# Kernel optimization log

Hardware: AMD Instinct MI355X
Metric: run time of the kernel (lower is better)

## Reference

```python
import jax, jax.numpy as jnp
import numpy as np

N_NODES = 20000
N_EDGES = 160000
D_IN = 512
D_OUT = 64


def _propagate(x, src, dst, num_nodes):
    # SLPropagate with add_self_loops=False, normalize=False:
    # out[dst] += x[src]  (plain sum aggregation over incoming edges)
    return jax.ops.segment_sum(x[src], dst, num_segments=num_nodes)


def setup_inputs() -> dict:
    key = jax.random.key(0)
    k1, k2, k3, k4 = jax.random.split(key, 4)
    x = jax.random.normal(k1, (N_NODES, D_IN), dtype=jnp.float32)
    edge_index = jax.random.randint(k2, (2, N_EDGES), 0, N_NODES, dtype=jnp.int64)
    # torch.nn.Linear default init scale ~ 1/sqrt(fan_in)
    s = 1.0 / np.sqrt(D_IN)
    W1 = jax.random.uniform(k3, (D_IN, D_IN), dtype=jnp.float32, minval=-s, maxval=s)
    W2 = jax.random.uniform(k4, (D_OUT, D_IN), dtype=jnp.float32, minval=-s, maxval=s)
    return {"x": x, "edge_index": edge_index, "W1": W1, "W2": W2}


def reference(x, edge_index, W1, W2):
    num_nodes = x.shape[0]
    src, dst = edge_index[0], edge_index[1]
    h = _propagate(x, src, dst, num_nodes)          # [N, D_IN]
    h = jax.nn.relu(jnp.einsum('nd,ed->ne', h, W1))  # lin1 (no bias) + relu
    h = _propagate(h, src, dst, num_nodes)          # [N, D_IN]
    h = jnp.einsum('nd,od->no', h, W2)              # lin2 (no bias) -> [N, D_OUT]
    return jax.nn.log_softmax(h, axis=1)
```

## Files before the change

kernel.cpp:

```cpp
#include <hip/hip_runtime.h>

#define D 512
#define DOUT 64

typedef __bf16 bf16x8 __attribute__((ext_vector_type(8)));
typedef float floatx4 __attribute__((ext_vector_type(4)));

__device__ __forceinline__ void async_cp16(const void* g, void* lds) {
    __builtin_amdgcn_global_load_lds(
        (__attribute__((address_space(1))) void*)(void*)g,
        (__attribute__((address_space(3))) void*)lds, 16, 0, 0);
}

__global__ __launch_bounds__(256) void prep_kernel(
        int* __restrict__ deg, int nN, int zeroBlocks,
        const float* __restrict__ x, __bf16* __restrict__ xb, int xN8,
        const float* __restrict__ W1, __bf16* __restrict__ w1b, int w1N8,
        const float* __restrict__ W2, __bf16* __restrict__ w2b, int w2N8) {
    int b = blockIdx.x;
    if (b < zeroBlocks) {
        int i4 = b * 1024 + threadIdx.x * 4;
        if (i4 + 3 < nN) *(int4*)(deg + i4) = make_int4(0, 0, 0, 0);
        else {
            if (i4 + 0 < nN) deg[i4 + 0] = 0;
            if (i4 + 1 < nN) deg[i4 + 1] = 0;
            if (i4 + 2 < nN) deg[i4 + 2] = 0;
        }
        return;
    }
    b -= zeroBlocks;
    int xBlocks = (xN8 + 255) >> 8;
    int w1Blocks = (w1N8 + 255) >> 8;
    const float* in; __bf16* outp; int n8;
    if (b < xBlocks) { in = x; outp = xb; n8 = xN8; }
    else if (b < xBlocks + w1Blocks) { b -= xBlocks; in = W1; outp = w1b; n8 = w1N8; }
    else { b -= xBlocks + w1Blocks; in = W2; outp = w2b; n8 = w2N8; }
    int i = b * 256 + threadIdx.x;
    if (i < n8) {
        const float4* p = (const float4*)in + (size_t)i * 2;
        float4 v0 = p[0], v1 = p[1];
        bf16x8 o;
        o[0] = (__bf16)v0.x; o[1] = (__bf16)v0.y; o[2] = (__bf16)v0.z; o[3] = (__bf16)v0.w;
        o[4] = (__bf16)v1.x; o[5] = (__bf16)v1.y; o[6] = (__bf16)v1.z; o[7] = (__bf16)v1.w;
        *((bf16x8*)outp + i) = o;
    }
}

__global__ __launch_bounds__(1024) void exscan_kernel(const int* __restrict__ deg,
                                                      int* __restrict__ rp,
                                                      int* __restrict__ cursor, int n) {
    __shared__ int wtot[16];
    __shared__ int carry;
    int tid = threadIdx.x, lane = tid & 63, wid = tid >> 6;
    if (tid == 0) carry = 0;
    __syncthreads();
    for (int base = 0; base < n; base += 4096) {
        int i4 = base + tid * 4;
        int4 v = make_int4(0, 0, 0, 0);
        if (i4 + 3 < n) v = *(const int4*)(deg + i4);
        else {
            if (i4 + 0 < n) v.x = deg[i4 + 0];
            if (i4 + 1 < n) v.y = deg[i4 + 1];
            if (i4 + 2 < n) v.z = deg[i4 + 2];
            if (i4 + 3 < n) v.w = deg[i4 + 3];
        }
        int tsum = v.x + v.y + v.z + v.w;
        int s = tsum;
        #pragma unroll
        for (int off = 1; off < 64; off <<= 1) {
            int t = __shfl_up(s, off, 64);
            if (lane >= off) s += t;
        }
        if (lane == 63) wtot[wid] = s;
        __syncthreads();
        if (wid == 0 && lane < 16) {
            int wv = wtot[lane];
            int ws_ = wv;
            #pragma unroll
            for (int off = 1; off < 16; off <<= 1) {
                int t = __shfl_up(ws_, off, 64);
                if (lane >= off) ws_ += t;
            }
            wtot[lane] = ws_ - wv;
        }
        __syncthreads();
        int excl = carry + wtot[wid] + (s - tsum);
        int4 o;
        o.x = excl; o.y = o.x + v.x; o.z = o.y + v.y; o.w = o.z + v.z;
        if (i4 + 3 < n) {
            *(int4*)(rp + i4) = o;
            *(int4*)(cursor + i4) = o;
        } else {
            if (i4 + 0 < n) { rp[i4 + 0] = o.x; cursor[i4 + 0] = o.x; }
            if (i4 + 1 < n) { rp[i4 + 1] = o.y; cursor[i4 + 1] = o.y; }
            if (i4 + 2 < n) { rp[i4 + 2] = o.z; cursor[i4 + 2] = o.z; }
            if (i4 + 3 < n) { rp[i4 + 3] = o.w; cursor[i4 + 3] = o.w; }
        }
        __syncthreads();
        if (tid == 1023) carry = o.w + v.w;
        __syncthreads();
    }
    if (tid == 0) rp[n] = carry;
}

__global__ void fill_kernel(const int* __restrict__ src, const int* __restrict__ dst,
                            int* __restrict__ cursor, int* __restrict__ col, int nE) {
    int e = blockIdx.x * blockDim.x + threadIdx.x;
    if (e < nE) {
        int d = dst[e];
        int p = atomicAdd(&cursor[d], 1);
        col[p] = src[e];
    }
}

__global__ __launch_bounds__(256) void gemm1_hist(
        const __bf16* __restrict__ A, const __bf16* __restrict__ B,
        __bf16* __restrict__ Cout, int M, int gemmBlocks,
        const int* __restrict__ dst, int* __restrict__ deg, int nE) {
    constexpr int BM = 128, BN = 128, BK = 32;
    constexpr int MI = 4, NI = 4;
    constexpr int CPA = 2, CPB = 2;

    if (blockIdx.x >= gemmBlocks) {
        int base = (blockIdx.x - gemmBlocks) * 256 + threadIdx.x;
        int stride = (gridDim.x - gemmBlocks) * 256;
        for (int e = base; e < nE; e += stride) atomicAdd(&deg[dst[e]], 1);
        return;
    }

    __shared__ __bf16 As[4 * BM * 8];
    __shared__ __bf16 Bs[4 * BN * 8];

    const int tid = threadIdx.x;
    const int w = tid >> 6, lane = tid & 63;
    const int wrow = w >> 1, wcol = w & 1;
    const int m0 = (blockIdx.x >> 2) * BM, n0 = (blockIdx.x & 3) * BN;
    const int quad = lane >> 4, l15 = lane & 15;

    floatx4 acc[MI][NI] = {};

    for (int k0 = 0; k0 < D; k0 += BK) {
        #pragma unroll
        for (int c = 0; c < CPA; ++c) {
            int ca = w * CPA + c;
            int kq = ca / CPA;
            int row = m0 + (ca % CPA) * 64 + lane;
            if (row > M - 1) row = M - 1;
            async_cp16(A + (size_t)row * D + k0 + kq * 8, &As[(size_t)ca * 512]);
        }
        #pragma unroll
        for (int c = 0; c < CPB; ++c) {
            int cb = w * CPB + c;
            int kq = cb / CPB;
            int nn = n0 + (cb % CPB) * 64 + lane;
            async_cp16(B + (size_t)nn * D + k0 + kq * 8, &Bs[(size_t)cb * 512]);
        }
        __syncthreads();

        bf16x8 af[MI], bfr[NI];
        #pragma unroll
        for (int mi = 0; mi < MI; ++mi)
            af[mi] = *(const bf16x8*)&As[(size_t)(quad * BM + wrow * 64 + mi * 16 + l15) * 8];
        #pragma unroll
        for (int nj = 0; nj < NI; ++nj)
            bfr[nj] = *(const bf16x8*)&Bs[(size_t)(quad * BN + wcol * 64 + nj * 16 + l15) * 8];
        #pragma unroll
        for (int mi = 0; mi < MI; ++mi)
            #pragma unroll
            for (int nj = 0; nj < NI; ++nj)
                acc[mi][nj] = __builtin_amdgcn_mfma_f32_16x16x32_bf16(
                    af[mi], bfr[nj], acc[mi][nj], 0, 0, 0);
        __syncthreads();
    }

    #pragma unroll
    for (int mi = 0; mi < MI; ++mi) {
        #pragma unroll
        for (int r = 0; r < 4; ++r) {
            int m = m0 + wrow * 64 + mi * 16 + quad * 4 + r;
            if (m < M) {
                #pragma unroll
                for (int nj = 0; nj < NI; ++nj) {
                    int n = n0 + wcol * 64 + nj * 16 + l15;
                    Cout[(size_t)m * D + n] = (__bf16)acc[mi][nj][r];
                }
            }
        }
    }
}

__global__ __launch_bounds__(256) void prop1_gemm2(
        const __bf16* __restrict__ t, const int* __restrict__ rp,
        const int* __restrict__ col, const __bf16* __restrict__ B,
        __bf16* __restrict__ u, int nN) {
    __shared__ __bf16 As[16 * 512];
    __shared__ __bf16 Bs[4 * 64 * 8];

    const int tid = threadIdx.x;
    const int w = tid >> 6, lane = tid & 63;
    const int quad = lane >> 4, l15 = lane & 15;
    const int m0 = blockIdx.x * 16;

    for (int r = w; r < 16; r += 4) {
        int n = m0 + r;
        float acc0[8] = {}, acc1[8] = {};
        if (n < nN) {
            int s0 = rp[n], s1 = rp[n + 1];
            int e = s0;
            for (; e + 4 <= s1; e += 4) {
                int sa = col[e], sb = col[e + 1], sc = col[e + 2], sd = col[e + 3];
                bf16x8 va = *(const bf16x8*)(t + (size_t)sa * D + lane * 8);
                bf16x8 vb = *(const bf16x8*)(t + (size_t)sb * D + lane * 8);
                bf16x8 vc = *(const bf16x8*)(t + (size_t)sc * D + lane * 8);
                bf16x8 vd = *(const bf16x8*)(t + (size_t)sd * D + lane * 8);
                #pragma unroll
                for (int i = 0; i < 8; ++i) {
                    acc0[i] += (float)va[i] + (float)vc[i];
                    acc1[i] += (float)vb[i] + (float)vd[i];
                }
            }
            for (; e < s1; ++e) {
                int sa = col[e];
                bf16x8 va = *(const bf16x8*)(t + (size_t)sa * D + lane * 8);
                #pragma unroll
                for (int i = 0; i < 8; ++i) acc0[i] += (float)va[i];
            }
        }
        bf16x8 o;
        #pragma unroll
        for (int i = 0; i < 8; ++i) o[i] = (__bf16)fmaxf(acc0[i] + acc1[i], 0.f);
        int P = r * 64 + ((lane + r) & 63);
        *(bf16x8*)&As[(size_t)P * 8] = o;
    }
    __syncthreads();

    floatx4 acc = {};
    for (int k0 = 0; k0 < D; k0 += 32) {
        async_cp16(B + (size_t)lane * D + k0 + w * 8, &Bs[(size_t)w * 512]);
        __syncthreads();
        int g = (k0 >> 3) + quad;
        bf16x8 af = *(const bf16x8*)&As[(size_t)(l15 * 64 + ((g + l15) & 63)) * 8];
        bf16x8 bfr = *(const bf16x8*)&Bs[(size_t)(quad * 64 + w * 16 + l15) * 8];
        acc = __builtin_amdgcn_mfma_f32_16x16x32_bf16(af, bfr, acc, 0, 0, 0);
        __syncthreads();
    }

    #pragma unroll
    for (int r = 0; r < 4; ++r) {
        int m = m0 + quad * 4 + r;
        if (m < nN)
            u[(size_t)m * DOUT + w * 16 + l15] = (__bf16)acc[r];
    }
}

__global__ __launch_bounds__(256) void prop2_lsm(const __bf16* __restrict__ u,
        const int* __restrict__ rp, const int* __restrict__ col,
        float* __restrict__ out, int nN) {
    int n = blockIdx.x * 4 + (threadIdx.x >> 6);
    if (n >= nN) return;
    int lane = threadIdx.x & 63;
    int s0 = rp[n], s1 = rp[n + 1];
    float a0 = 0.f, a1 = 0.f, a2 = 0.f, a3 = 0.f;
    int e = s0;
    for (; e + 4 <= s1; e += 4) {
        int sa = col[e], sb = col[e + 1], sc = col[e + 2], sd = col[e + 3];
        a0 += (float)u[(size_t)sa * DOUT + lane];
        a1 += (float)u[(size_t)sb * DOUT + lane];
        a2 += (float)u[(size_t)sc * DOUT + lane];
        a3 += (float)u[(size_t)sd * DOUT + lane];
    }
    for (; e < s1; ++e) a0 += (float)u[(size_t)col[e] * DOUT + lane];
    float v = (a0 + a2) + (a1 + a3);
    float mx = v;
    #pragma unroll
    for (int off = 32; off >= 1; off >>= 1) mx = fmaxf(mx, __shfl_xor(mx, off, 64));
    float s = expf(v - mx);
    #pragma unroll
    for (int off = 32; off >= 1; off >>= 1) s += __shfl_xor(s, off, 64);
    out[(size_t)n * DOUT + lane] = v - mx - logf(s);
}


extern "C" void kernel_launch(void* const* d_in, const int* in_sizes, int n_in,
                              void* d_out, int out_size, void* d_ws, size_t ws_size,
                              hipStream_t stream) {
    const float* x  = (const float*)d_in[0];
    const int*   ei = (const int*)d_in[1];
    const float* W1 = (const float*)d_in[2];
    const float* W2 = (const float*)d_in[3];
    float* out = (float*)d_out;

    const int N = in_sizes[0] / D;
    const int E = in_sizes[1] / 2;
    const int* src = ei;
    const int* dst = ei + E;

    size_t off = 0;
    auto alloc = [&](size_t bytes) -> void* {
        void* p = (char*)d_ws + off;
        off = (off + bytes + 255) & ~(size_t)255;
        return p;
    };
    int*    deg     = (int*)alloc(sizeof(int) * (size_t)N);
    int*    row_ptr = (int*)alloc(sizeof(int) * (size_t)(N + 1));
    int*    cursor  = (int*)alloc(sizeof(int) * (size_t)N);
    int*    col     = (int*)alloc(sizeof(int) * (size_t)E);
    __bf16* w1b     = (__bf16*)alloc(sizeof(__bf16) * (size_t)D * D);
    __bf16* w2b     = (__bf16*)alloc(sizeof(__bf16) * (size_t)DOUT * D);
    __bf16* xb      = (__bf16*)alloc(sizeof(__bf16) * (size_t)N * D);
    __bf16* t       = (__bf16*)alloc(sizeof(__bf16) * (size_t)N * D);
    __bf16* u       = (__bf16*)alloc(sizeof(__bf16) * (size_t)N * DOUT);

    const int zeroBlocks = (N + 1023) / 1024;
    const int xN8 = N * D / 8, w1N8 = D * D / 8, w2N8 = DOUT * D / 8;
    const int cvtBlocks = (xN8 + 255) / 256 + (w1N8 + 255) / 256 + (w2N8 + 255) / 256;

    prep_kernel<<<zeroBlocks + cvtBlocks, 256, 0, stream>>>(
        deg, N, zeroBlocks, x, xb, xN8, W1, w1b, w1N8, W2, w2b, w2N8);

    const int gemmBlocks = ((N + 127) / 128) * 4;
    gemm1_hist<<<gemmBlocks + 64, 256, 0, stream>>>(
        xb, w1b, t, N, gemmBlocks, dst, deg, E);

    exscan_kernel<<<1, 1024, 0, stream>>>(deg, row_ptr, cursor, N);
    fill_kernel<<<(E + 255) / 256, 256, 0, stream>>>(src, dst, cursor, col, E);

    prop1_gemm2<<<(N + 15) / 16, 256, 0, stream>>>(t, row_ptr, col, w2b, u, N);
    prop2_lsm<<<(N + 3) / 4, 256, 0, stream>>>(u, row_ptr, col, out, N);
}
```

Baseline: 175.7 us.

## Fuse bf16 conversion into GEMM loads and merge scan with CSR fill

Removes the separate fp32-to-bf16 prep kernel: gemm1 now loads fp32 x and W1 directly, converts to bf16 in registers and stores into LDS, and prop1_gemm2 converts W2 on the fly. The single-block exclusive scan and the fill kernel are merged into one launch that uses a decoupled-lookback style multi-block scan with release/acquire flags, and fill blocks spin until all scan blocks publish. Degree and flag zeroing moves to a memset. This avoids writing and rereading a bf16 copy of x and saves launches, but gives up the async global-to-LDS copies, doubles gemm1 global read bytes, and relies on scan blocks being scheduled before the spinning fill blocks.

Result: slower. 250.8 us (+42.7%).

```diff
diff --git a/kernel.cpp b/kernel.cpp
--- a/kernel.cpp
+++ b/kernel.cpp
@@ -2,132 +2,36 @@
 
 #define D 512
 #define DOUT 64
+#define TAG (1 << 30)
 
 typedef __bf16 bf16x8 __attribute__((ext_vector_type(8)));
 typedef float floatx4 __attribute__((ext_vector_type(4)));
 
-__device__ __forceinline__ void async_cp16(const void* g, void* lds) {
-    __builtin_amdgcn_global_load_lds(
-        (__attribute__((address_space(1))) void*)(void*)g,
-        (__attribute__((address_space(3))) void*)lds, 16, 0, 0);
-}
-
-__global__ __launch_bounds__(256) void prep_kernel(
-        int* __restrict__ deg, int nN, int zeroBlocks,
-        const float* __restrict__ x, __bf16* __restrict__ xb, int xN8,
-        const float* __restrict__ W1, __bf16* __restrict__ w1b, int w1N8,
-        const float* __restrict__ W2, __bf16* __restrict__ w2b, int w2N8) {
-    int b = blockIdx.x;
-    if (b < zeroBlocks) {
-        int i4 = b * 1024 + threadIdx.x * 4;
-        if (i4 + 3 < nN) *(int4*)(deg + i4) = make_int4(0, 0, 0, 0);
-        else {
-            if (i4 + 0 < nN) deg[i4 + 0] = 0;
-            if (i4 + 1 < nN) deg[i4 + 1] = 0;
-            if (i4 + 2 < nN) deg[i4 + 2] = 0;
-        }
-        return;
-    }
-    b -= zeroBlocks;
-    int xBlocks = (xN8 + 255) >> 8;
-    int w1Blocks = (w1N8 + 255) >> 8;
-    const float* in; __bf16* outp; int n8;
-    if (b < xBlocks) { in = x; outp = xb; n8 = xN8; }
-    else if (b < xBlocks + w1Blocks) { b -= xBlocks; in = W1; outp = w1b; n8 = w1N8; }
-    else { b -= xBlocks + w1Blocks; in = W2; outp = w2b; n8 = w2N8; }
-    int i = b * 256 + threadIdx.x;
-    if (i < n8) {
-        const float4* p = (const float4*)in + (size_t)i * 2;
-        float4 v0 = p[0], v1 = p[1];
-        bf16x8 o;
-        o[0] = (__bf16)v0.x; o[1] = (__bf16)v0.y; o[2] = (__bf16)v0.z; o[3] = (__bf16)v0.w;
-        o[4] = (__bf16)v1.x; o[5] = (__bf16)v1.y; o[6] = (__bf16)v1.z; o[7] = (__bf16)v1.w;
-        *((bf16x8*)outp + i) = o;
-    }
-}
-
-__global__ __launch_bounds__(1024) void exscan_kernel(const int* __restrict__ deg,
-                                                      int* __restrict__ rp,
-                                                      int* __restrict__ cursor, int n) {
-    __shared__ int wtot[16];
-    __shared__ int carry;
-    int tid = threadIdx.x, lane = tid & 63, wid = tid >> 6;
-    if (tid == 0) carry = 0;
-    __syncthreads();
-    for (int base = 0; base < n; base += 4096) {
-        int i4 = base + tid * 4;
-        int4 v = make_int4(0, 0, 0, 0);
-        if (i4 + 3 < n) v = *(const int4*)(deg + i4);
-        else {
-            if (i4 + 0 < n) v.x = deg[i4 + 0];
-            if (i4 + 1 < n) v.y = deg[i4 + 1];
-            if (i4 + 2 < n) v.z = deg[i4 + 2];
-            if (i4 + 3 < n) v.w = deg[i4 + 3];
-        }
-        int tsum = v.x + v.y + v.z + v.w;
-        int s = tsum;
-        #pragma unroll
-        for (int off = 1; off < 64; off <<= 1) {
-            int t = __shfl_up(s, off, 64);
-            if (lane >= off) s += t;
-        }
-        if (lane == 63) wtot[wid] = s;
-        __syncthreads();
-        if (wid == 0 && lane < 16) {
-            int wv = wtot[lane];
-            int ws_ = wv;
-            #pragma unroll
-            for (int off = 1; off < 16; off <<= 1) {
-                int t = __shfl_up(ws_, off, 64);
-                if (lane >= off) ws_ += t;
-            }
-            wtot[lane] = ws_ - wv;
-        }
-        __syncthreads();
-        int excl = carry + wtot[wid] + (s - tsum);
-        int4 o;
-        o.x = excl; o.y = o.x + v.x; o.z = o.y + v.y; o.w = o.z + v.z;
-        if (i4 + 3 < n) {
-            *(int4*)(rp + i4) = o;
-            *(int4*)(cursor + i4) = o;
-        } else {
-            if (i4 + 0 < n) { rp[i4 + 0] = o.x; cursor[i4 + 0] = o.x; }
-            if (i4 + 1 < n) { rp[i4 + 1] = o.y; cursor[i4 + 1] = o.y; }
-            if (i4 + 2 < n) { rp[i4 + 2] = o.z; cursor[i4 + 2] = o.z; }
-            if (i4 + 3 < n) { rp[i4 + 3] = o.w; cursor[i4 + 3] = o.w; }
-        }
-        __syncthreads();
-        if (tid == 1023) carry = o.w + v.w;
-        __syncthreads();
-    }
-    if (tid == 0) rp[n] = carry;
-}
-
-__global__ void fill_kernel(const int* __restrict__ src, const int* __restrict__ dst,
-                            int* __restrict__ cursor, int* __restrict__ col, int nE) {
-    int e = blockIdx.x * blockDim.x + threadIdx.x;
-    if (e < nE) {
-        int d = dst[e];
-        int p = atomicAdd(&cursor[d], 1);
-        col[p] = src[e];
-    }
+__device__ __forceinline__ bf16x8 cvt8f(float4 a0, float4 a1) {
+    bf16x8 o;
+    o[0] = (__bf16)a0.x; o[1] = (__bf16)a0.y; o[2] = (__bf16)a0.z; o[3] = (__bf16)a0.w;
+    o[4] = (__bf16)a1.x; o[5] = (__bf16)a1.y; o[6] = (__bf16)a1.z; o[7] = (__bf16)a1.w;
+    return o;
+}
+
+__device__ __forceinline__ int ld_acq(int* p) {
+    return __hip_atomic_load(p, __ATOMIC_ACQUIRE, __HIP_MEMORY_SCOPE_AGENT);
+}
+__device__ __forceinline__ void st_rel(int* p, int v) {
+    __hip_atomic_store(p, v, __ATOMIC_RELEASE, __HIP_MEMORY_SCOPE_AGENT);
 }
 
 __global__ __launch_bounds__(256) void gemm1_hist(
-        const __bf16* __restrict__ A, const __bf16* __restrict__ B,
+        const float* __restrict__ A, const float* __restrict__ Bw,
         __bf16* __restrict__ Cout, int M, int gemmBlocks,
         const int* __restrict__ dst, int* __restrict__ deg, int nE) {
-    constexpr int BM = 128, BN = 128, BK = 32;
-    constexpr int MI = 4, NI = 4;
-    constexpr int CPA = 2, CPB = 2;
-
     if (blockIdx.x >= gemmBlocks) {
         int base = (blockIdx.x - gemmBlocks) * 256 + threadIdx.x;
         int stride = (gridDim.x - gemmBlocks) * 256;
         for (int e = base; e < nE; e += stride) atomicAdd(&deg[dst[e]], 1);
         return;
     }
-
+    constexpr int BM = 128, BN = 128, BK = 32;
     __shared__ __bf16 As[4 * BM * 8];
     __shared__ __bf16 Bs[4 * BN * 8];
 
@@ -137,50 +41,47 @@
     const int m0 = (blockIdx.x >> 2) * BM, n0 = (blockIdx.x & 3) * BN;
     const int quad = lane >> 4, l15 = lane & 15;
 
-    floatx4 acc[MI][NI] = {};
+    floatx4 acc[4][4] = {};
 
     for (int k0 = 0; k0 < D; k0 += BK) {
         #pragma unroll
-        for (int c = 0; c < CPA; ++c) {
-            int ca = w * CPA + c;
-            int kq = ca / CPA;
-            int row = m0 + (ca % CPA) * 64 + lane;
-            if (row > M - 1) row = M - 1;
-            async_cp16(A + (size_t)row * D + k0 + kq * 8, &As[(size_t)ca * 512]);
-        }
-        #pragma unroll
-        for (int c = 0; c < CPB; ++c) {
-            int cb = w * CPB + c;
-            int kq = cb / CPB;
-            int nn = n0 + (cb % CPB) * 64 + lane;
-            async_cp16(B + (size_t)nn * D + k0 + kq * 8, &Bs[(size_t)cb * 512]);
-        }
-        __syncthreads();
-
-        bf16x8 af[MI], bfr[NI];
-        #pragma unroll
-        for (int mi = 0; mi < MI; ++mi)
+        for (int gi = 0; gi < 2; ++gi) {
+            int g = tid + gi * 256;
+            int kq = g >> 7, row = g & 127;
+            int ar = m0 + row; if (ar > M - 1) ar = M - 1;
+            const float4* ap = (const float4*)(A + (size_t)ar * D + k0 + kq * 8);
+            float4 a0 = ap[0], a1 = ap[1];
+            const float4* bp = (const float4*)(Bw + (size_t)(n0 + row) * D + k0 + kq * 8);
+            float4 b0 = bp[0], b1 = bp[1];
+            *(bf16x8*)&As[(size_t)g * 8] = cvt8f(a0, a1);
+            *(bf16x8*)&Bs[(size_t)g * 8] = cvt8f(b0, b1);
+        }
+        __syncthreads();
+
+        bf16x8 af[4], bfr[4];
+        #pragma unroll
+        for (int mi = 0; mi < 4; ++mi)
             af[mi] = *(const bf16x8*)&As[(size_t)(quad * BM + wrow * 64 + mi * 16 + l15) * 8];
         #pragma unroll
-        for (int nj = 0; nj < NI; ++nj)
+        for (int nj = 0; nj < 4; ++nj)
             bfr[nj] = *(const bf16x8*)&Bs[(size_t)(quad * BN + wcol * 64 + nj * 16 + l15) * 8];
         #pragma unroll
-        for (int mi = 0; mi < MI; ++mi)
+        for (int mi = 0; mi < 4; ++mi)
             #pragma unroll
-            for (int nj = 0; nj < NI; ++nj)
+            for (int nj = 0; nj < 4; ++nj)
                 acc[mi][nj] = __builtin_amdgcn_mfma_f32_16x16x32_bf16(
                     af[mi], bfr[nj], acc[mi][nj], 0, 0, 0);
         __syncthreads();
     }
 
     #pragma unroll
-    for (int mi = 0; mi < MI; ++mi) {
+    for (int mi = 0; mi < 4; ++mi) {
         #pragma unroll
         for (int r = 0; r < 4; ++r) {
             int m = m0 + wrow * 64 + mi * 16 + quad * 4 + r;
             if (m < M) {
                 #pragma unroll
-                for (int nj = 0; nj < NI; ++nj) {
+                for (int nj = 0; nj < 4; ++nj) {
                     int n = n0 + wcol * 64 + nj * 16 + l15;
                     Cout[(size_t)m * D + n] = (__bf16)acc[mi][nj][r];
                 }
@@ -189,9 +90,87 @@
     }
 }
 
+__global__ __launch_bounds__(256) void scanfill_kernel(
+        const int* __restrict__ deg, int* __restrict__ rp, int* __restrict__ cursor,
+        int* __restrict__ col, const int* __restrict__ src, const int* __restrict__ dst,
+        int* __restrict__ prefix, int* __restrict__ sflag, int nN, int nE, int SB) {
+    const int tid = threadIdx.x, b = blockIdx.x;
+    const int lane = tid & 63, wid = tid >> 6;
+
+    if (b < SB) {
+        __shared__ int wtot[4];
+        __shared__ int s_prev;
+        int i4 = b * 1024 + tid * 4;
+        int4 v = make_int4(0, 0, 0, 0);
+        if (i4 + 3 < nN) v = *(const int4*)(deg + i4);
+        else {
+            if (i4 + 0 < nN) v.x = deg[i4 + 0];
+            if (i4 + 1 < nN) v.y = deg[i4 + 1];
+            if (i4 + 2 < nN) v.z = deg[i4 + 2];
+        }
+        int tsum = v.x + v.y + v.z + v.w;
+        int s = tsum;
+        #pragma unroll
+        for (int off = 1; off < 64; off <<= 1) {
+            int t = __shfl_up(s, off, 64);
+            if (lane >= off) s += t;
+        }
+        if (lane == 63) wtot[wid] = s;
+        __syncthreads();
+        int woff = 0, btot = 0;
+        #pragma unroll
+        for (int i = 0; i < 4; ++i) {
+            if (i < wid) woff += wtot[i];
+            btot += wtot[i];
+        }
+        if (tid == 0) st_rel(&prefix[b], TAG | btot);
+        if (tid < 64) {
+            int myv = 0;
+            if (tid < b) {
+                int vv;
+                while (((vv = ld_acq(&prefix[tid])) & TAG) == 0)
+                    __builtin_amdgcn_s_sleep(1);
+                myv = vv & (TAG - 1);
+            }
+            #pragma unroll
+            for (int off = 32; off >= 1; off >>= 1) myv += __shfl_xor(myv, off, 64);
+            if (tid == 0) s_prev = myv;
+        }
+        __syncthreads();
+        int prevsum = s_prev;
+        int excl = prevsum + woff + (s - tsum);
+        int4 o;
+        o.x = excl; o.y = o.x + v.x; o.z = o.y + v.y; o.w = o.z + v.z;
+        if (i4 + 3 < nN) {
+            *(int4*)(rp + i4) = o;
+            *(int4*)(cursor + i4) = o;
+        } else {
+            if (i4 + 0 < nN) { rp[i4 + 0] = o.x; cursor[i4 + 0] = o.x; }
+            if (i4 + 1 < nN) { rp[i4 + 1] = o.y; cursor[i4 + 1] = o.y; }
+            if (i4 + 2 < nN) { rp[i4 + 2] = o.z; cursor[i4 + 2] = o.z; }
+        }
+        if (tid == 0 && b == SB - 1) rp[nN] = prevsum + btot;
+        __threadfence();
+        __syncthreads();
+        if (tid == 0) st_rel(&sflag[b], TAG);
+    } else {
+        if (tid < SB) {
+            while ((ld_acq(&sflag[tid]) & TAG) == 0)
+                __builtin_amdgcn_s_sleep(2);
+        }
+        __syncthreads();
+        int e = (b - SB) * 256 + tid;
+        if (e < nE) {
+            int d = dst[e];
+            int p = atomicAdd(&cursor[d], 1);
+            col[p] = src[e];
+        }
+    }
+}
+
 __global__ __launch_bounds__(256) void prop1_gemm2(
         const __bf16* __restrict__ t, const int* __restrict__ rp,
-        const int* __restrict__ col, const __bf16* __restrict__ B,
+        const int* __restrict__ col, const float* __restrict__ W2f,
         __bf16* __restrict__ u, int nN) {
     __shared__ __bf16 As[16 * 512];
     __shared__ __bf16 Bs[4 * 64 * 8];
@@ -236,7 +215,9 @@
 
     floatx4 acc = {};
     for (int k0 = 0; k0 < D; k0 += 32) {
-        async_cp16(B + (size_t)lane * D + k0 + w * 8, &Bs[(size_t)w * 512]);
+        const float4* bp = (const float4*)(W2f + (size_t)lane * D + k0 + w * 8);
+        float4 b0 = bp[0], b1 = bp[1];
+        *(bf16x8*)&Bs[(size_t)tid * 8] = cvt8f(b0, b1);
         __syncthreads();
         int g = (k0 >> 3) + quad;
         bf16x8 af = *(const bf16x8*)&As[(size_t)(l15 * 64 + ((g + l15) & 63)) * 8];
@@ -294,6 +275,7 @@
     const int E = in_sizes[1] / 2;
     const int* src = ei;
     const int* dst = ei + E;
+    const int SB = (N + 1023) / 1024;
 
     size_t off = 0;
     auto alloc = [&](size_t bytes) -> void* {
@@ -301,30 +283,26 @@
         off = (off + bytes + 255) & ~(size_t)255;
         return p;
     };
-    int*    deg     = (int*)alloc(sizeof(int) * (size_t)N);
+    int*    meta    = (int*)alloc(sizeof(int) * (size_t)(N + 2 * SB));
+    int*    deg     = meta;
+    int*    prefix  = meta + N;
+    int*    sflag   = meta + N + SB;
     int*    row_ptr = (int*)alloc(sizeof(int) * (size_t)(N + 1));
     int*    cursor  = (int*)alloc(sizeof(int) * (size_t)N);
     int*    col     = (int*)alloc(sizeof(int) * (size_t)E);
-    __bf16* w1b     = (__bf16*)alloc(sizeof(__bf16) * (size_t)D * D);
-    __bf16* w2b     = (__bf16*)alloc(sizeof(__bf16) * (size_t)DOUT * D);
-    __bf16* xb      = (__bf16*)alloc(sizeof(__bf16) * (size_t)N * D);
     __bf16* t       = (__bf16*)alloc(sizeof(__bf16) * (size_t)N * D);
     __bf16* u       = (__bf16*)alloc(sizeof(__bf16) * (size_t)N * DOUT);
 
-    const int zeroBlocks = (N + 1023) / 1024;
-    const int xN8 = N * D / 8, w1N8 = D * D / 8, w2N8 = DOUT * D / 8;
-    const int cvtBlocks = (xN8 + 255) / 256 + (w1N8 + 255) / 256 + (w2N8 + 255) / 256;
-
-    prep_kernel<<<zeroBlocks + cvtBlocks, 256, 0, stream>>>(
-        deg, N, zeroBlocks, x, xb, xN8, W1, w1b, w1N8, W2, w2b, w2N8);
+    hipMemsetAsync(meta, 0, sizeof(int) * (size_t)(N + 2 * SB), stream);
 
     const int gemmBlocks = ((N + 127) / 128) * 4;
-    gemm1_hist<<<gemmBlocks + 64, 256, 0, stream>>>(
-        xb, w1b, t, N, gemmBlocks, dst, deg, E);
-
-    exscan_kernel<<<1, 1024, 0, stream>>>(deg, row_ptr, cursor, N);
-    fill_kernel<<<(E + 255) / 256, 256, 0, stream>>>(src, dst, cursor, col, E);
-
-    prop1_gemm2<<<(N + 15) / 16, 256, 0, stream>>>(t, row_ptr, col, w2b, u, N);
+    gemm1_hist<<<gemmBlocks + 64, 256, 0, stream>>>(x, W1, t, N, gemmBlocks, dst, deg, E);
+
+    const int fillBlocks = (E + 255) / 256;
+    scanfill_kernel<<<SB + fillBlocks, 256, 0, stream>>>(
+        deg, row_ptr, cursor, col, src, dst, prefix, sflag, N, E, SB);
+
+    prop1_gemm2<<<(N + 15) / 16, 256, 0, stream>>>(t, row_ptr, col, W2, u, N);
+
     prop2_lsm<<<(N + 3) / 4, 256, 0, stream>>>(u, row_ptr, col, out, N);
 }
```
